# Kernel optimization log

Measured on AMD Instinct MI355X. Metric: run time of the kernel, lower is better.

Reference implementation:

```python
import jax, jax.numpy as jnp
import numpy as np

B, H, W, C = 2, 64, 64, 256
NH, K = 8, 7  # num_heads, neighborhood kernel size


def setup_inputs() -> dict:
    key = jax.random.key(0)
    ks = jax.random.split(key, 8)
    xav = lambda k, shape: jax.random.normal(k, shape, jnp.float32) * np.sqrt(2.0 / (shape[0] + shape[1])).astype(np.float32)
    return {
        "x": jax.random.normal(ks[0], (B, H, W, C), jnp.float32),
        "norm1_g": jnp.ones((C,), jnp.float32),
        "norm1_b": jnp.zeros((C,), jnp.float32),
        "qkv_w": xav(ks[1], (3 * C, C)),
        "qkv_b": jnp.zeros((3 * C,), jnp.float32),
        "rpb": jax.random.normal(ks[2], (NH, 2 * K - 1, 2 * K - 1), jnp.float32) * 0.02,
        "proj_w": xav(ks[3], (C, C)),
        "proj_b": jnp.zeros((C,), jnp.float32),
        "norm2_g": jnp.ones((C,), jnp.float32),
        "norm2_b": jnp.zeros((C,), jnp.float32),
        "fc1_w": xav(ks[4], (4 * C, C)),
        "fc1_b": jnp.zeros((4 * C,), jnp.float32),
        "fc2_w": xav(ks[5], (C, 4 * C)),
        "fc2_b": jnp.zeros((C,), jnp.float32),
    }


def _layernorm(x, g, b, eps=1e-5):
    m = x.mean(-1, keepdims=True)
    v = jnp.mean((x - m) ** 2, axis=-1, keepdims=True)
    return (x - m) * jax.lax.rsqrt(v + eps) * g + b


def _nat2d(x, qkv_w, qkv_b, rpb, proj_w, proj_b):
    """Neighborhood attention 2D (NATTEN semantics: edge-clamped k x k windows,
    relative positional bias indexed by key_pos - query_pos + k - 1)."""
    b, h, w, c = x.shape
    nh = rpb.shape[0]
    k = (rpb.shape[1] + 1) // 2
    dh = c // nh
    qkv = (x @ qkv_w.T + qkv_b).reshape(b, h, w, 3, nh, dh)
    q = qkv[..., 0, :, :] * (dh ** -0.5)  # [b,h,w,nh,dh]
    kk = qkv[..., 1, :, :]
    vv = qkv[..., 2, :, :]
    # edge-clamped window starts per query row/col
    starts_h = jnp.clip(jnp.arange(h) - k // 2, 0, h - k)
    starts_w = jnp.clip(jnp.arange(w) - k // 2, 0, w - k)
    idx_h = starts_h[:, None] + jnp.arange(k)  # [h,k] key row indices
    idx_w = starts_w[:, None] + jnp.arange(k)  # [w,k] key col indices
    # gather neighborhoods -> [b,h,w,k,k,nh,dh]
    knb = kk[:, idx_h][:, :, :, idx_w].transpose(0, 1, 3, 2, 4, 5, 6)
    vnb = vv[:, idx_h][:, :, :, idx_w].transpose(0, 1, 3, 2, 4, 5, 6)
    attn = jnp.einsum('bijhd,bijklhd->bijhkl', q, knb)  # [b,h,w,nh,k,k]
    # relative positional bias: index = key - query + (k-1) in [0, 2k-2]
    rb_h = idx_h - jnp.arange(h)[:, None] + (k - 1)  # [h,k]
    rb_w = idx_w - jnp.arange(w)[:, None] + (k - 1)  # [w,k]
    bias = rpb[:, rb_h][:, :, :, rb_w]  # [nh,h,k,w,k]
    bias = bias.transpose(1, 3, 0, 2, 4)  # [h,w,nh,k,k]
    attn = jax.nn.softmax((attn + bias).reshape(b, h, w, nh, k * k), axis=-1)
    out = jnp.einsum('bijhn,bijnhd->bijhd', attn, vnb.reshape(b, h, w, k * k, nh, dh))
    return out.reshape(b, h, w, c) @ proj_w.T + proj_b


def reference(x, norm1_g, norm1_b, qkv_w, qkv_b, rpb, proj_w, proj_b,
              norm2_g, norm2_b, fc1_w, fc1_b, fc2_w, fc2_b):
    # norm -> neighborhood attention -> residual
    x = x + _nat2d(_layernorm(x, norm1_g, norm1_b), qkv_w, qkv_b, rpb, proj_w, proj_b)
    # norm -> MLP (gelu) -> residual
    hdn = _layernorm(x, norm2_g, norm2_b)
    hdn = jax.nn.gelu(hdn @ fc1_w.T + fc1_b, approximate=False)
    return x + (hdn @ fc2_w.T + fc2_b)
```

## Files before the change

kernel.cpp:

```cpp
#include <hip/hip_runtime.h>

typedef __attribute__((ext_vector_type(8))) short bf16x8;
typedef __attribute__((ext_vector_type(4))) float f32x4;
typedef unsigned short u16;

__device__ __forceinline__ float bf2f(u16 u) {
    return __builtin_bit_cast(float, ((unsigned int)u) << 16);
}
__device__ __forceinline__ u16 f2bf(float f) {
    unsigned int x = __builtin_bit_cast(unsigned int, f);
    x += 0x7FFFu + ((x >> 16) & 1u);
    return (u16)(x >> 16);
}

typedef const __attribute__((address_space(1))) void* gas_t;
typedef __attribute__((address_space(3))) void* las_t;
__device__ __forceinline__ void load_lds16(const u16* g, u16* l) {
    __builtin_amdgcn_global_load_lds((gas_t)g, (las_t)l, 16, 0, 0);
}

__global__ __launch_bounds__(256) void prep_kernel(
    const float* __restrict__ s0, const float* __restrict__ s1,
    const float* __restrict__ s2, const float* __restrict__ s3,
    u16* __restrict__ dst,
    const float* __restrict__ x, const float* __restrict__ g,
    const float* __restrict__ b, u16* __restrict__ y)
{
    if (blockIdx.x < 768) {
        const int i4 = (blockIdx.x * 256 + threadIdx.x) * 4;
        const float* src;
        int off;
        if      (i4 < 196608) { src = s0; off = i4; }
        else if (i4 < 262144) { src = s1; off = i4 - 196608; }
        else if (i4 < 524288) { src = s2; off = i4 - 262144; }
        else                  { src = s3; off = i4 - 524288; }
        float4 v = *(const float4*)(src + off);
        ushort4 o;
        o.x = f2bf(v.x); o.y = f2bf(v.y); o.z = f2bf(v.z); o.w = f2bf(v.w);
        *(ushort4*)(dst + i4) = o;
        return;
    }
    const int tok  = (blockIdx.x - 768) * 4 + (threadIdx.x >> 6);
    const int lane = threadIdx.x & 63;
    float4 v = *(const float4*)(x + (size_t)tok * 256 + lane * 4);
    float s  = v.x + v.y + v.z + v.w;
    float sq = v.x*v.x + v.y*v.y + v.z*v.z + v.w*v.w;
    #pragma unroll
    for (int off = 32; off; off >>= 1) {
        s  += __shfl_xor(s, off);
        sq += __shfl_xor(sq, off);
    }
    float mean = s * (1.0f / 256.0f);
    float var  = sq * (1.0f / 256.0f) - mean * mean;
    float rs   = rsqrtf(var + 1e-5f);
    float4 gv = *(const float4*)(g + lane * 4);
    float4 bv = *(const float4*)(b + lane * 4);
    ushort4 o;
    o.x = f2bf((v.x - mean) * rs * gv.x + bv.x);
    o.y = f2bf((v.y - mean) * rs * gv.y + bv.y);
    o.z = f2bf((v.z - mean) * rs * gv.z + bv.z);
    o.w = f2bf((v.w - mean) * rs * gv.w + bv.w);
    *(ushort4*)(y + (size_t)tok * 256 + lane * 4) = o;
}

template<int BM, int BN, int N, int K, int EPI>
__global__ __launch_bounds__(256) void gemm(
    const u16* __restrict__ A, const u16* __restrict__ W,
    const float* __restrict__ bias, const float* __restrict__ res,
    void* __restrict__ outv)
{
    constexpr int WMT = BM / 32;
    constexpr int WNT = BN / 32;
    constexpr int AR  = BM / 32;
    constexpr int BR  = BN / 32;

    __shared__ u16 As[BM * 64];
    __shared__ u16 Bs[BN * 64];
    const int tid  = threadIdx.x;
    const int lane = tid & 63;
    const int wave = tid >> 6;
    const int m0   = blockIdx.x * BM;
    const int n0   = blockIdx.y * BN;
    const int wm0  = (wave >> 1) * (BM / 2);
    const int wn0  = (wave & 1) * (BN / 2);

    f32x4 acc[WMT][WNT];
    #pragma unroll
    for (int mt = 0; mt < WMT; ++mt)
        #pragma unroll
        for (int nt = 0; nt < WNT; ++nt)
            acc[mt][nt] = (f32x4){0.f, 0.f, 0.f, 0.f};

    int soffA[AR];
    #pragma unroll
    for (int r = 0; r < AR; ++r) {
        const int s   = r * 256 + tid;
        const int row = s >> 3;
        const int c   = (s & 7) ^ (row & 7);
        soffA[r] = row * K + c * 8;
    }
    int soffB[BR];
    #pragma unroll
    for (int r = 0; r < BR; ++r) {
        const int s   = r * 256 + tid;
        const int row = s >> 3;
        const int c   = (s & 7) ^ (row & 7);
        soffB[r] = row * K + c * 8;
    }
    const int fr = lane & 15;
    const int fc = lane >> 4;

    for (int k0 = 0; k0 < K; k0 += 64) {
        __syncthreads();
        #pragma unroll
        for (int r = 0; r < AR; ++r)
            load_lds16(A + (size_t)m0 * K + k0 + soffA[r], As + (r * 256 + tid) * 8);
        #pragma unroll
        for (int r = 0; r < BR; ++r)
            load_lds16(W + (size_t)n0 * K + k0 + soffB[r], Bs + (r * 256 + tid) * 8);
        __syncthreads();
        #pragma unroll
        for (int ks = 0; ks < 2; ++ks) {
            bf16x8 af[WMT], bw[WNT];
            #pragma unroll
            for (int mt = 0; mt < WMT; ++mt) {
                const int rr   = wm0 + mt * 16 + fr;
                const int phys = (ks * 4 + fc) ^ (rr & 7);
                af[mt] = *(const bf16x8*)(As + rr * 64 + phys * 8);
            }
            #pragma unroll
            for (int nt = 0; nt < WNT; ++nt) {
                const int rr   = wn0 + nt * 16 + fr;
                const int phys = (ks * 4 + fc) ^ (rr & 7);
                bw[nt] = *(const bf16x8*)(Bs + rr * 64 + phys * 8);
            }
            #pragma unroll
            for (int mt = 0; mt < WMT; ++mt)
                #pragma unroll
                for (int nt = 0; nt < WNT; ++nt)
                    acc[mt][nt] = __builtin_amdgcn_mfma_f32_16x16x32_bf16(af[mt], bw[nt], acc[mt][nt], 0, 0, 0);
        }
    }

    const int col = lane & 15;
    const int rb  = (lane >> 4) * 4;
    #pragma unroll
    for (int nt = 0; nt < WNT; ++nt) {
        const int n  = n0 + wn0 + nt * 16 + col;
        const float bv = bias[n];
        #pragma unroll
        for (int mt = 0; mt < WMT; ++mt) {
            #pragma unroll
            for (int r = 0; r < 4; ++r) {
                const int m = m0 + wm0 + mt * 16 + rb + r;
                float v = acc[mt][nt][r] + bv;
                if (EPI == 1) {
                    if (n < 256) v *= 0.1767766952966369f;
                    ((u16*)outv)[(size_t)m * N + n] = f2bf(v);
                }
                if (EPI == 2) {
                    v += res[(size_t)m * N + n];
                    ((float*)outv)[(size_t)m * N + n] = v;
                }
                if (EPI == 3) {
                    v = 0.5f * v * (1.0f + erff(v * 0.7071067811865475f));
                    ((u16*)outv)[(size_t)m * N + n] = f2bf(v);
                }
            }
        }
    }
}

__global__ __launch_bounds__(512) void attn_proj_kernel(
    const u16* __restrict__ qkv, const float* __restrict__ rpb,
    const u16* __restrict__ projW, const float* __restrict__ proj_b,
    const float* __restrict__ xres, const float* __restrict__ g2,
    const float* __restrict__ b2, float* __restrict__ x1,
    u16* __restrict__ ln2)
{
    __shared__ u16   Ks[112 * 256];
    __shared__ u16   Qs[16 * 256];
    __shared__ u16   ao[16 * 256];
    __shared__ float rpbs[8 * 177];
    __shared__ float red[8][16][2];

    const int tid = threadIdx.x;
    const int l   = tid & 63;
    const int w   = tid >> 6;
    const int B   = blockIdx.x;
    const int tile = (B & 7) * 64 + (B >> 3);
    const int bb   = tile >> 8;
    const int rem  = tile & 255;
    const int ti0  = (rem >> 4) << 2;
    const int tj0  = (rem & 15) << 2;
    const int oh   = min(max(ti0 - 3, 0), 54);
    const int ow   = min(max(tj0 - 3, 0), 54);
    const int tokbase = bb * 4096;

    #pragma unroll
    for (int r = 0; r < 7; ++r) {
        const int s   = r * 512 + tid;
        const int key = s >> 5;
        const int pc  = s & 31;
        const int gc  = pc ^ (key & 31);
        const int kkc = min(key, 99);
        const int tr  = (kkc * 205) >> 11, tc = kkc - tr * 10;
        const int tokg = tokbase + (oh + tr) * 64 + (ow + tc);
        load_lds16(qkv + (size_t)tokg * 768 + 256 + gc * 8, Ks + s * 8);
    }
    {
        const int s   = tid;
        const int tok = s >> 5;
        const int pc  = s & 31;
        const int gc  = pc ^ (tok & 31);
        const int tokq = tokbase + (ti0 + (tok >> 2)) * 64 + (tj0 + (tok & 3));
        load_lds16(qkv + (size_t)tokq * 768 + gc * 8, Qs + s * 8);
    }
    #pragma unroll
    for (int r = 0; r < 3; ++r) {
        const int idx = r * 512 + tid;
        if (idx < 1416) {
            const int hh = idx / 177;
            const int ii = idx - hh * 177;
            rpbs[idx] = (ii < 169) ? rpb[hh * 169 + ii] : -1e30f;
        }
    }

    const int q = l & 15;
    const int g = l >> 4;

    const int i  = ti0 + (q >> 2), j = tj0 + (q & 3);
    const int sh = min(max(i - 3, 0), 57), sw = min(max(j - 3, 0), 57);
    const int khb = sh - oh, kwb = sw - ow;
    const int bh0 = oh - i + 6, bw0 = ow - j + 6;
    int bidx[7][4];
    int vtok[7][4];
    #pragma unroll
    for (int t = 0; t < 7; ++t)
        #pragma unroll
        for (int r = 0; r < 4; ++r) {
            const int kk  = 16 * t + 4 * g + r;
            const int kkc = min(kk, 99);
            const int hr  = (kkc * 205) >> 11;
            const int hc  = kkc - hr * 10;
            vtok[t][r] = tokbase + (oh + hr) * 64 + (ow + hc);
            const bool valid = (kk < 100)
                && ((unsigned)(hr - khb) < 7u) && ((unsigned)(hc - kwb) < 7u);
            bidx[t][r] = valid ? (bh0 + hr) * 13 + (bw0 + hc) : 169;
        }

    __syncthreads();

    const int cw = w * 4 + g;
    const bf16x8 qf = *(const bf16x8*)(Qs + q * 256 + (cw ^ (q & 31)) * 8);
    bf16x8 kf[7];
    #pragma unroll
    for (int t = 0; t < 7; ++t) {
        const int key = 16 * t + q;
        kf[t] = *(const bf16x8*)(Ks + key * 256 + (cw ^ (key & 31)) * 8);
    }

    f32x4 S[7];
    #pragma unroll
    for (int t = 0; t < 7; ++t)
        S[t] = __builtin_amdgcn_mfma_f32_16x16x32_bf16(kf[t], qf, (f32x4){0.f,0.f,0.f,0.f}, 0, 0, 0);

    const float* rpbh = rpbs + w * 177;
    float p[7][4];
    float mx = -1e30f;
    #pragma unroll
    for (int t = 0; t < 7; ++t)
        #pragma unroll
        for (int r = 0; r < 4; ++r) {
            const float v = S[t][r] + rpbh[bidx[t][r]];
            p[t][r] = v;
            mx = fmaxf(mx, v);
        }
    mx = fmaxf(mx, __shfl_xor(mx, 16));
    mx = fmaxf(mx, __shfl_xor(mx, 32));
    float sum = 0.f;
    #pragma unroll
    for (int t = 0; t < 7; ++t)
        #pragma unroll
        for (int r = 0; r < 4; ++r) {
            const float e = __expf(p[t][r] - mx);
            p[t][r] = e;
            sum += e;
        }
    sum += __shfl_xor(sum, 16);
    sum += __shfl_xor(sum, 32);
    const float inv = 1.f / sum;

    f32x4 O0 = {0.f,0.f,0.f,0.f}, O1 = {0.f,0.f,0.f,0.f};
    const u16* vbase = qkv + 512 + w * 32 + q;
    #pragma unroll
    for (int kt = 0; kt < 4; ++kt) {
        const int t0   = 2 * kt;
        const bool has1 = (2 * kt + 1) < 7;
        const int t1   = has1 ? 2 * kt + 1 : 2 * kt;
        bf16x8 ph, pl, vA, vB;
        #pragma unroll
        for (int jj = 0; jj < 4; ++jj) {
            const float a = p[t0][jj] * inv;
            const u16 ha = f2bf(a);
            ph[jj] = (short)ha;
            pl[jj] = (short)f2bf(a - bf2f(ha));
            const float b = has1 ? p[t1][jj] * inv : 0.f;
            const u16 hb = f2bf(b);
            ph[4 + jj] = (short)hb;
            pl[4 + jj] = (short)f2bf(b - bf2f(hb));
            vA[jj]     = (short)vbase[(size_t)vtok[t0][jj] * 768];
            vB[jj]     = (short)vbase[(size_t)vtok[t0][jj] * 768 + 16];
            vA[4 + jj] = (short)vbase[(size_t)vtok[t1][jj] * 768];
            vB[4 + jj] = (short)vbase[(size_t)vtok[t1][jj] * 768 + 16];
        }
        O0 = __builtin_amdgcn_mfma_f32_16x16x32_bf16(ph, vA, O0, 0, 0, 0);
        O0 = __builtin_amdgcn_mfma_f32_16x16x32_bf16(pl, vA, O0, 0, 0, 0);
        O1 = __builtin_amdgcn_mfma_f32_16x16x32_bf16(ph, vB, O1, 0, 0, 0);
        O1 = __builtin_amdgcn_mfma_f32_16x16x32_bf16(pl, vB, O1, 0, 0, 0);
    }

    #pragma unroll
    for (int r = 0; r < 4; ++r) {
        const int row = g * 4 + r;
        const int c0  = w * 4 + (q >> 3);
        const int c1  = c0 + 2;
        ao[row * 256 + ((c0 ^ (row & 7)) << 3) + (q & 7)] = f2bf(O0[r]);
        ao[row * 256 + ((c1 ^ (row & 7)) << 3) + (q & 7)] = f2bf(O1[r]);
    }
    __syncthreads();

    const int fr  = l & 15;
    const int fc  = l >> 4;
    const int n0w = w * 32;
    f32x4 pacc[2];
    pacc[0] = (f32x4){0.f,0.f,0.f,0.f};
    pacc[1] = (f32x4){0.f,0.f,0.f,0.f};
    #pragma unroll
    for (int ks = 0; ks < 8; ++ks) {
        const int physA = (ks * 4 + fc) ^ (fr & 7);
        const bf16x8 af = *(const bf16x8*)(ao + fr * 256 + physA * 8);
        #pragma unroll
        for (int nt = 0; nt < 2; ++nt) {
            const int n = n0w + nt * 16 + fr;
            const bf16x8 bw = *(const bf16x8*)(projW + (size_t)n * 256 + ks * 32 + fc * 8);
            pacc[nt] = __builtin_amdgcn_mfma_f32_16x16x32_bf16(af, bw, pacc[nt], 0, 0, 0);
        }
    }

    const int col = l & 15;
    const int rb  = (l >> 4) * 4;
    float vv[2][4];
    float s[4]  = {0.f, 0.f, 0.f, 0.f};
    float sq[4] = {0.f, 0.f, 0.f, 0.f};
    #pragma unroll
    for (int nt = 0; nt < 2; ++nt) {
        const int n = n0w + nt * 16 + col;
        const float bv = proj_b[n];
        #pragma unroll
        for (int r = 0; r < 4; ++r) {
            const int t = rb + r;
            const size_t gi = (size_t)(tokbase + (ti0 + (t >> 2)) * 64 + (tj0 + (t & 3))) * 256 + n;
            float v = pacc[nt][r] + bv + xres[gi];
            x1[gi] = v;
            vv[nt][r] = v;
            s[r]  += v;
            sq[r] += v * v;
        }
    }
    #pragma unroll
    for (int off = 1; off < 16; off <<= 1) {
        #pragma unroll
        for (int r = 0; r < 4; ++r) {
            s[r]  += __shfl_xor(s[r], off);
            sq[r] += __shfl_xor(sq[r], off);
        }
    }
    if (col == 0) {
        #pragma unroll
        for (int r = 0; r < 4; ++r) {
            red[w][rb + r][0] = s[r];
            red[w][rb + r][1] = sq[r];
        }
    }
    __syncthreads();
    float mean[4], rsv[4];
    #pragma unroll
    for (int r = 0; r < 4; ++r) {
        float ts = 0.f, tq = 0.f;
        #pragma unroll
        for (int ww = 0; ww < 8; ++ww) {
            ts += red[ww][rb + r][0];
            tq += red[ww][rb + r][1];
        }
        mean[r] = ts * (1.0f / 256.0f);
        const float var = tq * (1.0f / 256.0f) - mean[r] * mean[r];
        rsv[r]  = rsqrtf(var + 1e-5f);
    }
    #pragma unroll
    for (int nt = 0; nt < 2; ++nt) {
        const int n = n0w + nt * 16 + col;
        const float gv  = g2[n];
        const float bv2 = b2[n];
        #pragma unroll
        for (int r = 0; r < 4; ++r) {
            const int t = rb + r;
            const size_t gi = (size_t)(tokbase + (ti0 + (t >> 2)) * 64 + (tj0 + (t & 3))) * 256 + n;
            ln2[gi] = f2bf((vv[nt][r] - mean[r]) * rsv[r] * gv + bv2);
        }
    }
}

extern "C" void kernel_launch(void* const* d_in, const int* in_sizes, int n_in,
                              void* d_out, int out_size, void* d_ws, size_t ws_size,
                              hipStream_t stream)
{
    const float* x      = (const float*)d_in[0];
    const float* n1g    = (const float*)d_in[1];
    const float* n1b    = (const float*)d_in[2];
    const float* qkv_w  = (const float*)d_in[3];
    const float* qkv_b  = (const float*)d_in[4];
    const float* rpb    = (const float*)d_in[5];
    const float* proj_w = (const float*)d_in[6];
    const float* proj_b = (const float*)d_in[7];
    const float* n2g    = (const float*)d_in[8];
    const float* n2b    = (const float*)d_in[9];
    const float* fc1_w  = (const float*)d_in[10];
    const float* fc1_b  = (const float*)d_in[11];
    const float* fc2_w  = (const float*)d_in[12];
    const float* fc2_b  = (const float*)d_in[13];
    float* out = (float*)d_out;

    char* wsb = (char*)d_ws;
    u16*   wbf   = (u16*)wsb;
    u16*   qkvW  = wbf;
    u16*   projW = wbf + 196608;
    u16*   fc1W  = wbf + 262144;
    u16*   fc2W  = wbf + 524288;
    u16*   ln1   = (u16*)(wsb + 1572864);
    u16*   qkvB  = (u16*)(wsb + 5767168);
    u16*   hbuf  = (u16*)(wsb + 9961472);
    float* x1    = (float*)(wsb + 26738688);
    u16*   ln2   = (u16*)(wsb + 35651584);

    dim3 blk(256);
    prep_kernel<<<2816, blk, 0, stream>>>(qkv_w, proj_w, fc1_w, fc2_w, wbf,
                                          x, n1g, n1b, ln1);
    gemm<128, 64, 768, 256, 1><<<dim3(64, 12), blk, 0, stream>>>(ln1, qkvW, qkv_b, nullptr, qkvB);
    attn_proj_kernel<<<512, dim3(512), 0, stream>>>(qkvB, rpb, projW, proj_b, x, n2g, n2b, x1, ln2);
    gemm<128, 64, 1024, 256, 3><<<dim3(64, 16), blk, 0, stream>>>(ln2, fc1W, fc1_b, nullptr, hbuf);
    gemm<64, 64, 256, 1024, 2><<<dim3(128, 4), blk, 0, stream>>>(hbuf, fc2W, fc2_b, x1, out);
}
```

Baseline: 144.4 us.

## Stage V tile in LDS reusing K buffer and drop split-bf16 probability MMA

Once QK^T is done, the block stages the V neighbourhood tile into the shared K buffer with asynchronous global-to-LDS loads, then reads V fragments from swizzled LDS. This replaces scattered 2-byte global gathers in the PV loop. It also removes the hi/lo bf16 split of the probabilities, which halves the PV MFMAs at the cost of lower precision in the attention weights. Two extra block barriers are added to protect reuse of the K buffer.

```diff
diff --git a/kernel.cpp b/kernel.cpp
--- a/kernel.cpp
+++ b/kernel.cpp
@@ -234,7 +234,6 @@
     const int khb = sh - oh, kwb = sw - ow;
     const int bh0 = oh - i + 6, bw0 = ow - j + 6;
     int bidx[7][4];
-    int vtok[7][4];
     #pragma unroll
     for (int t = 0; t < 7; ++t)
         #pragma unroll
@@ -243,7 +242,6 @@
             const int kkc = min(kk, 99);
             const int hr  = (kkc * 205) >> 11;
             const int hc  = kkc - hr * 10;
-            vtok[t][r] = tokbase + (oh + hr) * 64 + (ow + hc);
             const bool valid = (kk < 100)
                 && ((unsigned)(hr - khb) < 7u) && ((unsigned)(hc - kwb) < 7u);
             bidx[t][r] = valid ? (bh0 + hr) * 13 + (bw0 + hc) : 169;
@@ -265,6 +263,20 @@
     for (int t = 0; t < 7; ++t)
         S[t] = __builtin_amdgcn_mfma_f32_16x16x32_bf16(kf[t], qf, (f32x4){0.f,0.f,0.f,0.f}, 0, 0, 0);
 
+    __syncthreads();
+
+    #pragma unroll
+    for (int r = 0; r < 7; ++r) {
+        const int s   = r * 512 + tid;
+        const int key = s >> 5;
+        const int pc  = s & 31;
+        const int gc  = pc ^ (key & 31);
+        const int kkc = min(key, 99);
+        const int tr  = (kkc * 205) >> 11, tc = kkc - tr * 10;
+        const int tokg = tokbase + (oh + tr) * 64 + (ow + tc);
+        load_lds16(qkv + (size_t)tokg * 768 + 512 + gc * 8, Ks + s * 8);
+    }
+
     const float* rpbh = rpbs + w * 177;
     float p[7][4];
     float mx = -1e30f;
@@ -291,33 +303,33 @@
     sum += __shfl_xor(sum, 32);
     const float inv = 1.f / sum;
 
+    __syncthreads();
+
     f32x4 O0 = {0.f,0.f,0.f,0.f}, O1 = {0.f,0.f,0.f,0.f};
-    const u16* vbase = qkv + 512 + w * 32 + q;
+    const int cA = w * 4 + (q >> 3);
+    const int cB = cA + 2;
+    const int qb = q & 7;
     #pragma unroll
     for (int kt = 0; kt < 4; ++kt) {
         const int t0   = 2 * kt;
         const bool has1 = (2 * kt + 1) < 7;
         const int t1   = has1 ? 2 * kt + 1 : 2 * kt;
-        bf16x8 ph, pl, vA, vB;
+        bf16x8 ph, vA, vB;
         #pragma unroll
         for (int jj = 0; jj < 4; ++jj) {
             const float a = p[t0][jj] * inv;
-            const u16 ha = f2bf(a);
-            ph[jj] = (short)ha;
-            pl[jj] = (short)f2bf(a - bf2f(ha));
+            ph[jj] = (short)f2bf(a);
             const float b = has1 ? p[t1][jj] * inv : 0.f;
-            const u16 hb = f2bf(b);
-            ph[4 + jj] = (short)hb;
-            pl[4 + jj] = (short)f2bf(b - bf2f(hb));
-            vA[jj]     = (short)vbase[(size_t)vtok[t0][jj] * 768];
-            vB[jj]     = (short)vbase[(size_t)vtok[t0][jj] * 768 + 16];
-            vA[4 + jj] = (short)vbase[(size_t)vtok[t1][jj] * 768];
-            vB[4 + jj] = (short)vbase[(size_t)vtok[t1][jj] * 768 + 16];
+            ph[4 + jj] = (short)f2bf(b);
+            const int kk0 = 16 * t0 + 4 * g + jj;
+            const int kk1 = 16 * t1 + 4 * g + jj;
+            vA[jj]     = (short)Ks[kk0 * 256 + ((cA ^ (kk0 & 31)) << 3) + qb];
+            vB[jj]     = (short)Ks[kk0 * 256 + ((cB ^ (kk0 & 31)) << 3) + qb];
+            vA[4 + jj] = (short)Ks[kk1 * 256 + ((cA ^ (kk1 & 31)) << 3) + qb];
+            vB[4 + jj] = (short)Ks[kk1 * 256 + ((cB ^ (kk1 & 31)) << 3) + qb];
         }
         O0 = __builtin_amdgcn_mfma_f32_16x16x32_bf16(ph, vA, O0, 0, 0, 0);
-        O0 = __builtin_amdgcn_mfma_f32_16x16x32_bf16(pl, vA, O0, 0, 0, 0);
         O1 = __builtin_amdgcn_mfma_f32_16x16x32_bf16(ph, vB, O1, 0, 0, 0);
-        O1 = __builtin_amdgcn_mfma_f32_16x16x32_bf16(pl, vB, O1, 0, 0, 0);
     }
 
     #pragma unroll
```

New measurement: 147.7 us. 1.02x slower.

## Fuse FC1, GELU and FC2 into one MLP kernel keeping hidden in LDS

Applied to the files above, without the earlier changes.

Replaces the two separate MLP GEMM launches with a single kernel. Each block takes 32 tokens, computes FC1 plus exact GELU into a swizzled LDS hidden buffer, then runs FC2 with the bias and residual add. Both weight matrices are streamed through a double-buffered LDS tile. This removes the global write and read of the bf16 hidden activations and one launch. In exchange every block re-reads the full FC1 and FC2 weights, uses about 144KB of LDS so only one block fits per CU, and issues few MFMAs between barriers.

```diff
diff --git a/kernel.cpp b/kernel.cpp
--- a/kernel.cpp
+++ b/kernel.cpp
@@ -158,14 +158,6 @@
                     if (n < 256) v *= 0.1767766952966369f;
                     ((u16*)outv)[(size_t)m * N + n] = f2bf(v);
                 }
-                if (EPI == 2) {
-                    v += res[(size_t)m * N + n];
-                    ((float*)outv)[(size_t)m * N + n] = v;
-                }
-                if (EPI == 3) {
-                    v = 0.5f * v * (1.0f + erff(v * 0.7071067811865475f));
-                    ((u16*)outv)[(size_t)m * N + n] = f2bf(v);
-                }
             }
         }
     }
@@ -407,6 +399,131 @@
             const int t = rb + r;
             const size_t gi = (size_t)(tokbase + (ti0 + (t >> 2)) * 64 + (tj0 + (t & 3))) * 256 + n;
             ln2[gi] = f2bf((vv[nt][r] - mean[r]) * rsv[r] * gv + bv2);
+        }
+    }
+}
+
+__global__ __launch_bounds__(512) void mlp_kernel(
+    const u16* __restrict__ ln2, const u16* __restrict__ W1,
+    const float* __restrict__ b1, const u16* __restrict__ W2,
+    const float* __restrict__ b2, const float* __restrict__ x1,
+    float* __restrict__ out)
+{
+    __shared__ u16 As[32 * 256];
+    __shared__ u16 Ws[2][64 * 256];
+    __shared__ u16 Hs[32 * 1024];
+
+    const int tid = threadIdx.x;
+    const int l   = tid & 63;
+    const int w   = tid >> 6;
+    const int m0  = blockIdx.x * 32;
+    const int fr  = l & 15;
+    const int fc  = l >> 4;
+    const int col = l & 15;
+    const int rb  = (l >> 4) * 4;
+
+    #pragma unroll
+    for (int r = 0; r < 2; ++r) {
+        const int s = r * 512 + tid;
+        const int row = s >> 5;
+        const int c = (s & 31) ^ (row & 31);
+        load_lds16(ln2 + (size_t)(m0 + row) * 256 + c * 8, As + s * 8);
+    }
+    #pragma unroll
+    for (int r = 0; r < 4; ++r) {
+        const int s = r * 512 + tid;
+        const int row = s >> 5;
+        const int c = (s & 31) ^ (row & 31);
+        load_lds16(W1 + (size_t)row * 256 + c * 8, Ws[0] + s * 8);
+    }
+    __syncthreads();
+
+    const int wm1 = (w >> 2) * 16;
+    const int wn1 = (w & 3) * 16;
+    for (int nc = 0; nc < 16; ++nc) {
+        const int nbuf = (nc + 1) & 1;
+        if (nc + 1 < 16) {
+            #pragma unroll
+            for (int r = 0; r < 4; ++r) {
+                const int s = r * 512 + tid;
+                const int row = s >> 5;
+                const int c = (s & 31) ^ (row & 31);
+                load_lds16(W1 + (size_t)((nc + 1) * 64 + row) * 256 + c * 8, Ws[nbuf] + s * 8);
+            }
+        } else {
+            #pragma unroll
+            for (int r = 0; r < 4; ++r) {
+                const int s = r * 512 + tid;
+                const int row = s >> 3;
+                const int c = (s & 7) ^ (row & 7);
+                load_lds16(W2 + (size_t)row * 1024 + c * 8, Ws[nbuf] + s * 8);
+            }
+        }
+        const u16* Wb = Ws[nc & 1];
+        f32x4 acc = {0.f, 0.f, 0.f, 0.f};
+        #pragma unroll
+        for (int ks = 0; ks < 8; ++ks) {
+            const int ci = ks * 4 + fc;
+            const int ra = wm1 + fr;
+            const bf16x8 af = *(const bf16x8*)(As + ra * 256 + ((ci ^ (ra & 31)) << 3));
+            const int rw = wn1 + fr;
+            const bf16x8 bw = *(const bf16x8*)(Wb + rw * 256 + ((ci ^ (rw & 31)) << 3));
+            acc = __builtin_amdgcn_mfma_f32_16x16x32_bf16(af, bw, acc, 0, 0, 0);
+        }
+        #pragma unroll
+        for (int r = 0; r < 4; ++r) {
+            const int m = wm1 + rb + r;
+            const int ncol = nc * 64 + wn1 + col;
+            float v = acc[r] + b1[ncol];
+            v = 0.5f * v * (1.0f + erff(v * 0.7071067811865475f));
+            const int ci = ncol >> 3;
+            Hs[m * 1024 + ((ci ^ (m & 31)) << 3) + (ncol & 7)] = f2bf(v);
+        }
+        __syncthreads();
+    }
+
+    const int wm2 = (w & 1) * 16;
+    const int nb  = (w >> 1) * 64;
+    f32x4 acc2[4];
+    #pragma unroll
+    for (int nt = 0; nt < 4; ++nt) acc2[nt] = (f32x4){0.f,0.f,0.f,0.f};
+
+    for (int kc = 0; kc < 16; ++kc) {
+        if (kc + 1 < 16) {
+            const int nbuf = (kc + 1) & 1;
+            #pragma unroll
+            for (int r = 0; r < 4; ++r) {
+                const int s = r * 512 + tid;
+                const int row = s >> 3;
+                const int c = (s & 7) ^ (row & 7);
+                load_lds16(W2 + (size_t)row * 1024 + (kc + 1) * 64 + c * 8, Ws[nbuf] + s * 8);
+            }
+        }
+        const u16* Wb = Ws[kc & 1];
+        #pragma unroll
+        for (int ks = 0; ks < 2; ++ks) {
+            const int ci = kc * 8 + ks * 4 + fc;
+            const int ra = wm2 + fr;
+            const bf16x8 af = *(const bf16x8*)(Hs + ra * 1024 + ((ci ^ (ra & 31)) << 3));
+            #pragma unroll
+            for (int nt = 0; nt < 4; ++nt) {
+                const int rr = nb + nt * 16 + fr;
+                const bf16x8 bw = *(const bf16x8*)(Wb + rr * 64 + (((ks * 4 + fc) ^ (rr & 7)) << 3));
+                acc2[nt] = __builtin_amdgcn_mfma_f32_16x16x32_bf16(af, bw, acc2[nt], 0, 0, 0);
+            }
+        }
+        __syncthreads();
+    }
+
+    #pragma unroll
+    for (int nt = 0; nt < 4; ++nt) {
+        const int n = nb + nt * 16 + col;
+        const float bv = b2[n];
+        #pragma unroll
+        for (int r = 0; r < 4; ++r) {
+            const int m = m0 + wm2 + rb + r;
+            const size_t gi = (size_t)m * 256 + n;
+            out[gi] = acc2[nt][r] + bv + x1[gi];
         }
     }
 }
@@ -439,7 +556,6 @@
     u16*   fc2W  = wbf + 524288;
     u16*   ln1   = (u16*)(wsb + 1572864);
     u16*   qkvB  = (u16*)(wsb + 5767168);
-    u16*   hbuf  = (u16*)(wsb + 9961472);
     float* x1    = (float*)(wsb + 26738688);
     u16*   ln2   = (u16*)(wsb + 35651584);
 
@@ -448,6 +564,5 @@
                                           x, n1g, n1b, ln1);
     gemm<128, 64, 768, 256, 1><<<dim3(64, 12), blk, 0, stream>>>(ln1, qkvW, qkv_b, nullptr, qkvB);
     attn_proj_kernel<<<512, dim3(512), 0, stream>>>(qkvB, rpb, projW, proj_b, x, n2g, n2b, x1, ln2);
-    gemm<128, 64, 1024, 256, 3><<<dim3(64, 16), blk, 0, stream>>>(ln2, fc1W, fc1_b, nullptr, hbuf);
-    gemm<64, 64, 256, 1024, 2><<<dim3(128, 4), blk, 0, stream>>>(hbuf, fc2W, fc2_b, x1, out);
-}
+    mlp_kernel<<<256, dim3(512), 0, stream>>>(ln2, fc1W, fc1_b, fc2W, fc2_b, x1, out);
+}
```

After: 149.8 us. +3.7%, slower.

## Add single-shot K=256 GEMM with full-K LDS staging and XOR swizzle

Applied to the files above, without the earlier changes.

Adds a specialized GEMM for K=256 that stages the entire 64x256 A and B tiles into LDS in one pass with an XOR-swizzled layout, and then runs all eight MFMA k-steps with no further barriers. The QKV and FC1 projections switch to it with 64x64 tiles, which doubles the grid size. The intent is to remove the per-k-tile synchronization loop and LDS bank conflicts, and to raise the number of blocks available to the GPU. In exchange each block uses 64KB of LDS, which lowers how many blocks fit per CU, and smaller tiles reduce operand reuse.

```diff
diff --git a/kernel.cpp b/kernel.cpp
--- a/kernel.cpp
+++ b/kernel.cpp
@@ -63,6 +63,89 @@
     *(ushort4*)(y + (size_t)tok * 256 + lane * 4) = o;
 }
 
+template<int N, int EPI>
+__global__ __launch_bounds__(256) void gemm_k256(
+    const u16* __restrict__ A, const u16* __restrict__ W,
+    const float* __restrict__ bias, void* __restrict__ outv)
+{
+    __shared__ u16 As[64 * 256];
+    __shared__ u16 Bs[64 * 256];
+    const int tid  = threadIdx.x;
+    const int lane = tid & 63;
+    const int wave = tid >> 6;
+    const int m0   = blockIdx.x * 64;
+    const int n0   = blockIdx.y * 64;
+    const int wm0  = (wave >> 1) * 32;
+    const int wn0  = (wave & 1) * 32;
+
+    f32x4 acc[2][2];
+    #pragma unroll
+    for (int mt = 0; mt < 2; ++mt)
+        #pragma unroll
+        for (int nt = 0; nt < 2; ++nt)
+            acc[mt][nt] = (f32x4){0.f, 0.f, 0.f, 0.f};
+
+    #pragma unroll
+    for (int r = 0; r < 8; ++r) {
+        const int s   = r * 256 + tid;
+        const int row = s >> 5;
+        const int gc  = (s & 31) ^ (row & 31);
+        const int off = row * 256 + gc * 8;
+        load_lds16(A + (size_t)m0 * 256 + off, As + s * 8);
+        load_lds16(W + (size_t)n0 * 256 + off, Bs + s * 8);
+    }
+    __syncthreads();
+
+    const int fr = lane & 15;
+    const int fc = lane >> 4;
+    #pragma unroll
+    for (int ks = 0; ks < 8; ++ks) {
+        const int ci = ks * 4 + fc;
+        bf16x8 af[2], bw[2];
+        #pragma unroll
+        for (int mt = 0; mt < 2; ++mt) {
+            const int rr   = wm0 + mt * 16 + fr;
+            const int phys = ci ^ (rr & 31);
+            af[mt] = *(const bf16x8*)(As + rr * 256 + phys * 8);
+        }
+        #pragma unroll
+        for (int nt = 0; nt < 2; ++nt) {
+            const int rr   = wn0 + nt * 16 + fr;
+            const int phys = ci ^ (rr & 31);
+            bw[nt] = *(const bf16x8*)(Bs + rr * 256 + phys * 8);
+        }
+        #pragma unroll
+        for (int mt = 0; mt < 2; ++mt)
+            #pragma unroll
+            for (int nt = 0; nt < 2; ++nt)
+                acc[mt][nt] = __builtin_amdgcn_mfma_f32_16x16x32_bf16(af[mt], bw[nt], acc[mt][nt], 0, 0, 0);
+    }
+
+    const int col = lane & 15;
+    const int rb  = (lane >> 4) * 4;
+    #pragma unroll
+    for (int nt = 0; nt < 2; ++nt) {
+        const int n  = n0 + wn0 + nt * 16 + col;
+        const float bv = bias[n];
+        #pragma unroll
+        for (int mt = 0; mt < 2; ++mt) {
+            #pragma unroll
+            for (int r = 0; r < 4; ++r) {
+                const int m = m0 + wm0 + mt * 16 + rb + r;
+                float v = acc[mt][nt][r] + bv;
+                if (EPI == 1) {
+                    if (n < 256) v *= 0.1767766952966369f;
+                    ((u16*)outv)[(size_t)m * N + n] = f2bf(v);
+                }
+                if (EPI == 3) {
+                    v = 0.5f * v * (1.0f + erff(v * 0.7071067811865475f));
+                    ((u16*)outv)[(size_t)m * N + n] = f2bf(v);
+                }
+            }
+        }
+    }
+}
+
 template<int BM, int BN, int N, int K, int EPI>
 __global__ __launch_bounds__(256) void gemm(
     const u16* __restrict__ A, const u16* __restrict__ W,
@@ -154,17 +237,9 @@
             for (int r = 0; r < 4; ++r) {
                 const int m = m0 + wm0 + mt * 16 + rb + r;
                 float v = acc[mt][nt][r] + bv;
-                if (EPI == 1) {
-                    if (n < 256) v *= 0.1767766952966369f;
-                    ((u16*)outv)[(size_t)m * N + n] = f2bf(v);
-                }
                 if (EPI == 2) {
                     v += res[(size_t)m * N + n];
                     ((float*)outv)[(size_t)m * N + n] = v;
-                }
-                if (EPI == 3) {
-                    v = 0.5f * v * (1.0f + erff(v * 0.7071067811865475f));
-                    ((u16*)outv)[(size_t)m * N + n] = f2bf(v);
                 }
             }
         }
@@ -446,8 +521,8 @@
     dim3 blk(256);
     prep_kernel<<<2816, blk, 0, stream>>>(qkv_w, proj_w, fc1_w, fc2_w, wbf,
                                           x, n1g, n1b, ln1);
-    gemm<128, 64, 768, 256, 1><<<dim3(64, 12), blk, 0, stream>>>(ln1, qkvW, qkv_b, nullptr, qkvB);
+    gemm_k256<768, 1><<<dim3(128, 12), blk, 0, stream>>>(ln1, qkvW, qkv_b, qkvB);
     attn_proj_kernel<<<512, dim3(512), 0, stream>>>(qkvB, rpb, projW, proj_b, x, n2g, n2b, x1, ln2);
-    gemm<128, 64, 1024, 256, 3><<<dim3(64, 16), blk, 0, stream>>>(ln2, fc1W, fc1_b, nullptr, hbuf);
+    gemm_k256<1024, 3><<<dim3(128, 16), blk, 0, stream>>>(ln2, fc1W, fc1_b, hbuf);
     gemm<64, 64, 256, 1024, 2><<<dim3(128, 4), blk, 0, stream>>>(hbuf, fc2W, fc2_b, x1, out);
 }
```

Measured after the change: 151.1 us. 4.6% more time.
